# Performance work log

Hardware: AMD Instinct MI355X
Metric: run time of the kernel (lower is better)

Reference implementation:

```python
import jax, jax.numpy as jnp
import numpy as np

B, S, D, H, E, N = 4, 1024, 1024, 4096, 1024, 8


def setup_inputs() -> dict:
    key = jax.random.key(0)
    ks = jax.random.split(key, 5)
    x = jax.random.normal(ks[0], (B, S, D), jnp.float32)
    # Learned parameters (Linear weights stored as [in, out] for x @ W)
    Wg = jax.random.normal(ks[1], (D, N), jnp.float32) * 0.02
    bg = jnp.zeros((N,), jnp.float32)
    W1 = jax.random.normal(ks[2], (N, D, H), jnp.float32) * 0.02
    b1 = jnp.zeros((N, H), jnp.float32)
    W2 = jax.random.normal(ks[3], (N, H, E), jnp.float32) * 0.02
    b2 = jnp.zeros((N, E), jnp.float32)
    return {"x": x, "Wg": Wg, "bg": bg, "W1": W1, "b1": b1,
            "W2": W2, "b2": b2, "num_experts_per_tok": 2}


def reference(x, Wg, bg, W1, b1, W2, b2, num_experts_per_tok):
    # Gating: softmax over experts
    gate_probs = jax.nn.softmax(x @ Wg + bg, axis=-1)            # [B,S,N]
    n_exp = gate_probs.shape[-1]
    # Top-k routing mask (indices are distinct, so summed one-hots == scatter of 1.0)
    _, topk_idx = jax.lax.top_k(gate_probs, num_experts_per_tok)  # [B,S,k]
    mask = jax.nn.one_hot(topk_idx, n_exp, dtype=gate_probs.dtype).sum(axis=-2)  # [B,S,N]
    gated = gate_probs * mask
    # F.normalize(p=1): divide by max(L1-norm, eps)
    gated = gated / jnp.maximum(jnp.sum(jnp.abs(gated), axis=-1, keepdims=True), 1e-12)
    # Dense all-expert FFN (matches torch.stack over ModuleList)
    h = jax.nn.relu(jnp.einsum('bsd,ndh->bsnh', x, W1) + b1)      # [B,S,N,H]
    expert_out = jnp.einsum('bsnh,nhe->bsne', h, W2) + b2          # [B,S,N,E]
    out = jnp.einsum('bsn,bsne->bse', gated, expert_out)           # [B,S,E]
    # Auxiliary load-balancing stats
    tokens = float(x.shape[0] * x.shape[1])
    importance = gate_probs.sum(axis=(0, 1)) / tokens              # [N]
    load = mask.sum(axis=(0, 1)) / tokens                          # [N]
    lb_loss = (n_exp * (importance * load).sum()).astype(out.dtype)
    return out, lb_loss, importance, load
```

## Files before the change

### kernel.cpp

```cpp
#include <hip/hip_runtime.h>

#define TOKENS 4096
#define DDIM 1024
#define HDIM 4096
#define EDIM 1024
#define NEXP 8
#define SLOTS (TOKENS * 2)
#define OUT_MAIN ((size_t)TOKENS * EDIM)
#define NKC2 2
#define KCHUNK2 (HDIM / NKC2)

typedef __bf16 bf16_t;
typedef bf16_t bf16x8 __attribute__((ext_vector_type(8)));
typedef float f32x4 __attribute__((ext_vector_type(4)));

__device__ __forceinline__ unsigned short f32_to_bf16(float f) {
  union { float f; unsigned u; } v; v.f = f;
  unsigned r = v.u + 0x7FFFu + ((v.u >> 16) & 1u);
  return (unsigned short)(r >> 16);
}

__device__ __forceinline__ void gload_lds16(const void* g, void* l) {
  __builtin_amdgcn_global_load_lds(
      (__attribute__((address_space(1))) void*)(g),
      (__attribute__((address_space(3))) void*)(l), 16, 0, 0);
}

__global__ __launch_bounds__(256) void gate_kernel(
    const float* __restrict__ x, const float* __restrict__ Wg,
    const float* __restrict__ bg, unsigned short* __restrict__ xb,
    int2* __restrict__ tok_e, float2* __restrict__ tok_w,
    float* __restrict__ probs) {
  const int wave = threadIdx.x >> 6;
  const int lane = threadIdx.x & 63;
  const int t = blockIdx.x * 4 + wave;
  const float4* xr = reinterpret_cast<const float4*>(x + (size_t)t * DDIM);
  ushort4* xbr = reinterpret_cast<ushort4*>(xb + (size_t)t * DDIM);

  float acc[NEXP];
#pragma unroll
  for (int n = 0; n < NEXP; n++) acc[n] = 0.f;

#pragma unroll
  for (int i = 0; i < 4; i++) {
    int d4 = lane + 64 * i;
    float4 xv = xr[d4];
    ushort4 o;
    o.x = f32_to_bf16(xv.x); o.y = f32_to_bf16(xv.y);
    o.z = f32_to_bf16(xv.z); o.w = f32_to_bf16(xv.w);
    xbr[d4] = o;
    const float* wrow = Wg + (size_t)d4 * 4 * NEXP;
#pragma unroll
    for (int n = 0; n < NEXP; n++)
      acc[n] += xv.x * wrow[n] + xv.y * wrow[NEXP + n] +
                xv.z * wrow[2 * NEXP + n] + xv.w * wrow[3 * NEXP + n];
  }
#pragma unroll
  for (int n = 0; n < NEXP; n++)
#pragma unroll
    for (int m = 32; m > 0; m >>= 1) acc[n] += __shfl_xor(acc[n], m, 64);

  if (lane == 0) {
    float p[NEXP];
    float mx = -1e30f;
#pragma unroll
    for (int n = 0; n < NEXP; n++) { p[n] = acc[n] + bg[n]; mx = fmaxf(mx, p[n]); }
    float s = 0.f;
#pragma unroll
    for (int n = 0; n < NEXP; n++) { p[n] = expf(p[n] - mx); s += p[n]; }
    float inv = 1.f / s;
#pragma unroll
    for (int n = 0; n < NEXP; n++) { p[n] *= inv; probs[(size_t)t * NEXP + n] = p[n]; }
    int e1 = 0; float p1 = p[0];
#pragma unroll
    for (int n = 1; n < NEXP; n++) if (p[n] > p1) { p1 = p[n]; e1 = n; }
    int e2 = (e1 == 0) ? 1 : 0; float p2 = p[e2];
#pragma unroll
    for (int n = 0; n < NEXP; n++) if (n != e1 && p[n] > p2) { p2 = p[n]; e2 = n; }
    float denom = p1 + p2;
    tok_e[t] = make_int2(e1, e2);
    tok_w[t] = make_float2(p1 / denom, p2 / denom);
  }
}

__global__ __launch_bounds__(1024) void route_kernel(
    const int2* __restrict__ tok_e, const float2* __restrict__ tok_w,
    int* __restrict__ offs_g, int* __restrict__ counts_g,
    int* __restrict__ token_ids, float* __restrict__ slot_w) {
  __shared__ int cnt[NEXP];
  __shared__ int offs[NEXP + 1];
  __shared__ int cur[NEXP];
  const int tid = threadIdx.x;
  if (tid < NEXP) cnt[tid] = 0;
  __syncthreads();
  int2 e[4]; float2 w[4];
#pragma unroll
  for (int i = 0; i < 4; i++) {
    int t = tid + 1024 * i;
    e[i] = tok_e[t]; w[i] = tok_w[t];
    atomicAdd(&cnt[e[i].x], 1);
    atomicAdd(&cnt[e[i].y], 1);
  }
  __syncthreads();
  if (tid == 0) {
    int s = 0;
#pragma unroll
    for (int n = 0; n < NEXP; n++) { offs[n] = s; cur[n] = s; s += cnt[n]; }
    offs[NEXP] = s;
  }
  __syncthreads();
  if (tid < NEXP) { offs_g[tid] = offs[tid]; counts_g[tid] = cnt[tid]; }
  if (tid == 0) offs_g[NEXP] = offs[NEXP];
#pragma unroll
  for (int i = 0; i < 4; i++) {
    int t = tid + 1024 * i;
    int s0 = atomicAdd(&cur[e[i].x], 1);
    token_ids[s0] = t; slot_w[s0] = w[i].x;
    int s1 = atomicAdd(&cur[e[i].y], 1);
    token_ids[s1] = t; slot_w[s1] = w[i].y;
  }
}

__global__ __launch_bounds__(256) void transpose_convert_kernel(
    const float* __restrict__ src, unsigned short* __restrict__ dst, int R, int C) {
  __shared__ float tile[64][65];
  const size_t mat = (size_t)R * C;
  const float* s = src + (size_t)blockIdx.z * mat;
  unsigned short* d = dst + (size_t)blockIdx.z * mat;
  int c0 = blockIdx.x * 64, r0 = blockIdx.y * 64;
  int tx = threadIdx.x & 15, ty = threadIdx.x >> 4;
#pragma unroll
  for (int i = 0; i < 4; i++) {
    int row = ty + 16 * i;
    float4 v = *reinterpret_cast<const float4*>(&s[(size_t)(r0 + row) * C + c0 + tx * 4]);
    tile[row][tx * 4 + 0] = v.x;
    tile[row][tx * 4 + 1] = v.y;
    tile[row][tx * 4 + 2] = v.z;
    tile[row][tx * 4 + 3] = v.w;
  }
  __syncthreads();
#pragma unroll
  for (int i = 0; i < 4; i++) {
    int col = ty + 16 * i;
    ushort4 o;
    o.x = f32_to_bf16(tile[tx * 4 + 0][col]);
    o.y = f32_to_bf16(tile[tx * 4 + 1][col]);
    o.z = f32_to_bf16(tile[tx * 4 + 2][col]);
    o.w = f32_to_bf16(tile[tx * 4 + 3][col]);
    *reinterpret_cast<ushort4*>(&d[(size_t)(c0 + col) * R + r0 + tx * 4]) = o;
  }
}

__global__ __launch_bounds__(256) void gemm1_kernel(
    const unsigned short* __restrict__ xb, const unsigned short* __restrict__ w1t,
    const float* __restrict__ b1, const int* __restrict__ token_ids,
    const int* __restrict__ offs, unsigned short* __restrict__ h) {
  const int e = blockIdx.z;
  const int off0 = offs[e];
  const int ne = offs[e + 1] - off0;
  const int mt = blockIdx.y;
  if (mt * 128 >= ne) return;
  const int nt = blockIdx.x;

  __shared__ unsigned short As[2][128 * 64];
  __shared__ unsigned short Bs[2][128 * 64];

  const int tid = threadIdx.x;
  const int lane = tid & 63;
  const int wave = tid >> 6;
  const int wm = (wave >> 1) * 64;
  const int wn = (wave & 1) * 64;

  const int prow = tid >> 3;
  const int krow = (tid & 7) ^ (prow & 7);
  const unsigned short* gA[4];
  const unsigned short* gB[4];
  const unsigned short* wbase = w1t + (size_t)e * HDIM * DDIM;
#pragma unroll
  for (int j = 0; j < 4; j++) {
    int row = prow + j * 32;
    int slot = off0 + min(mt * 128 + row, ne - 1);
    gA[j] = xb + (size_t)token_ids[slot] * DDIM + krow * 8;
    gB[j] = wbase + (size_t)(nt * 128 + row) * DDIM + krow * 8;
  }

  f32x4 acc[4][4];
#pragma unroll
  for (int i = 0; i < 4; i++)
#pragma unroll
    for (int j = 0; j < 4; j++) acc[i][j] = (f32x4)(0.f);

  const int frow = lane & 15;
  const int q = lane >> 4;
  const int NK = DDIM / 64;

#pragma unroll
  for (int j = 0; j < 4; j++) {
    gload_lds16(gA[j], &As[0][j * 2048 + wave * 512]);
    gload_lds16(gB[j], &Bs[0][j * 2048 + wave * 512]);
  }
  __syncthreads();

  for (int t = 0; t < NK; t++) {
    const int cur = t & 1;
    if (t + 1 < NK) {
      const int k1 = (t + 1) * 64;
#pragma unroll
      for (int j = 0; j < 4; j++) {
        gload_lds16(gA[j] + k1, &As[cur ^ 1][j * 2048 + wave * 512]);
        gload_lds16(gB[j] + k1, &Bs[cur ^ 1][j * 2048 + wave * 512]);
      }
    }
#pragma unroll
    for (int kk = 0; kk < 2; kk++) {
      bf16x8 af[4], bfv[4];
#pragma unroll
      for (int mi = 0; mi < 4; mi++) {
        int row = wm + mi * 16 + frow;
        int k16 = (kk * 4 + q) ^ (row & 7);
        af[mi] = *reinterpret_cast<const bf16x8*>(&As[cur][row * 64 + k16 * 8]);
      }
#pragma unroll
      for (int ni = 0; ni < 4; ni++) {
        int row = wn + ni * 16 + frow;
        int k16 = (kk * 4 + q) ^ (row & 7);
        bfv[ni] = *reinterpret_cast<const bf16x8*>(&Bs[cur][row * 64 + k16 * 8]);
      }
#pragma unroll
      for (int mi = 0; mi < 4; mi++)
#pragma unroll
        for (int ni = 0; ni < 4; ni++)
          acc[mi][ni] = __builtin_amdgcn_mfma_f32_16x16x32_bf16(af[mi], bfv[ni], acc[mi][ni], 0, 0, 0);
    }
    __syncthreads();
  }

  const float* b1e = b1 + (size_t)e * HDIM + nt * 128;
  const int r4 = (lane >> 4) * 4;
  const int cb = lane & 15;
#pragma unroll
  for (int mi = 0; mi < 4; mi++) {
#pragma unroll
    for (int r = 0; r < 4; r++) {
      int grow = mt * 128 + wm + mi * 16 + r4 + r;
      if (grow < ne) {
        unsigned short* hr = h + (size_t)(off0 + grow) * HDIM + nt * 128;
#pragma unroll
        for (int ni = 0; ni < 4; ni++) {
          int col = wn + ni * 16 + cb;
          float v = acc[mi][ni][r] + b1e[col];
          hr[col] = f32_to_bf16(fmaxf(v, 0.f));
        }
      }
    }
  }
}

__global__ __launch_bounds__(256) void gemm2_kernel(
    const unsigned short* __restrict__ h, const unsigned short* __restrict__ w2t,
    const float* __restrict__ b2, const int* __restrict__ token_ids,
    const float* __restrict__ slot_w, const int* __restrict__ offs,
    float* __restrict__ out) {
  const int ez = blockIdx.z;
  const int e = ez >> 1;
  const int kc = ez & 1;
  const int off0 = offs[e];
  const int ne = offs[e + 1] - off0;
  const int mt = blockIdx.y;
  if (mt * 128 >= ne) return;
  const int nt = blockIdx.x;

  __shared__ unsigned short As[2][128 * 64];
  __shared__ unsigned short Bs[2][128 * 64];

  const int tid = threadIdx.x;
  const int lane = tid & 63;
  const int wave = tid >> 6;
  const int wm = (wave >> 1) * 64;
  const int wn = (wave & 1) * 64;

  const int prow = tid >> 3;
  const int krow = (tid & 7) ^ (prow & 7);
  const unsigned short* gA[4];
  const unsigned short* gB[4];
  const unsigned short* wbase = w2t + (size_t)e * EDIM * HDIM;
  const int kbase = kc * KCHUNK2;
#pragma unroll
  for (int j = 0; j < 4; j++) {
    int row = prow + j * 32;
    int slot = off0 + min(mt * 128 + row, ne - 1);
    gA[j] = h + (size_t)slot * HDIM + kbase + krow * 8;
    gB[j] = wbase + (size_t)(nt * 128 + row) * HDIM + kbase + krow * 8;
  }

  f32x4 acc[4][4];
#pragma unroll
  for (int i = 0; i < 4; i++)
#pragma unroll
    for (int j = 0; j < 4; j++) acc[i][j] = (f32x4)(0.f);

  const int frow = lane & 15;
  const int q = lane >> 4;
  const int NK = KCHUNK2 / 64;

#pragma unroll
  for (int j = 0; j < 4; j++) {
    gload_lds16(gA[j], &As[0][j * 2048 + wave * 512]);
    gload_lds16(gB[j], &Bs[0][j * 2048 + wave * 512]);
  }
  __syncthreads();

  for (int t = 0; t < NK; t++) {
    const int cur = t & 1;
    if (t + 1 < NK) {
      const int k1 = (t + 1) * 64;
#pragma unroll
      for (int j = 0; j < 4; j++) {
        gload_lds16(gA[j] + k1, &As[cur ^ 1][j * 2048 + wave * 512]);
        gload_lds16(gB[j] + k1, &Bs[cur ^ 1][j * 2048 + wave * 512]);
      }
    }
#pragma unroll
    for (int kk = 0; kk < 2; kk++) {
      bf16x8 af[4], bfv[4];
#pragma unroll
      for (int mi = 0; mi < 4; mi++) {
        int row = wm + mi * 16 + frow;
        int k16 = (kk * 4 + q) ^ (row & 7);
        af[mi] = *reinterpret_cast<const bf16x8*>(&As[cur][row * 64 + k16 * 8]);
      }
#pragma unroll
      for (int ni = 0; ni < 4; ni++) {
        int row = wn + ni * 16 + frow;
        int k16 = (kk * 4 + q) ^ (row & 7);
        bfv[ni] = *reinterpret_cast<const bf16x8*>(&Bs[cur][row * 64 + k16 * 8]);
      }
#pragma unroll
      for (int mi = 0; mi < 4; mi++)
#pragma unroll
        for (int ni = 0; ni < 4; ni++)
          acc[mi][ni] = __builtin_amdgcn_mfma_f32_16x16x32_bf16(af[mi], bfv[ni], acc[mi][ni], 0, 0, 0);
    }
    __syncthreads();
  }

  const float* b2e = b2 + (size_t)e * EDIM + nt * 128;
  const int r4 = (lane >> 4) * 4;
  const int cb = lane & 15;
#pragma unroll
  for (int mi = 0; mi < 4; mi++) {
#pragma unroll
    for (int r = 0; r < 4; r++) {
      int grow = mt * 128 + wm + mi * 16 + r4 + r;
      if (grow < ne) {
        int slot = off0 + grow;
        int tokid = token_ids[slot];
        float wgt = slot_w[slot];
        float* orow = out + (size_t)tokid * EDIM + nt * 128;
#pragma unroll
        for (int ni = 0; ni < 4; ni++) {
          int col = wn + ni * 16 + cb;
          float bias = (kc == 0) ? b2e[col] : 0.f;
          atomicAdd(&orow[col], (acc[mi][ni][r] + bias) * wgt);
        }
      }
    }
  }
}

__global__ __launch_bounds__(512) void stats_kernel(
    const float* __restrict__ probs, const int* __restrict__ counts,
    float* __restrict__ tail) {
  const int wave = threadIdx.x >> 6;
  const int lane = threadIdx.x & 63;
  float s = 0.f;
  for (int t = lane; t < TOKENS; t += 64) s += probs[(size_t)t * NEXP + wave];
#pragma unroll
  for (int m = 32; m > 0; m >>= 1) s += __shfl_xor(s, m, 64);
  __shared__ float imp_s[NEXP];
  if (lane == 0) imp_s[wave] = s / (float)TOKENS;
  __syncthreads();
  if (threadIdx.x == 0) {
    float lb = 0.f;
#pragma unroll
    for (int n = 0; n < NEXP; n++) {
      float imp = imp_s[n];
      float ld = (float)counts[n] / (float)TOKENS;
      tail[1 + n] = imp;
      tail[1 + NEXP + n] = ld;
      lb += imp * ld;
    }
    tail[0] = (float)NEXP * lb;
  }
}

extern "C" void kernel_launch(void* const* d_in, const int* in_sizes, int n_in,
                              void* d_out, int out_size, void* d_ws, size_t ws_size,
                              hipStream_t stream) {
  const float* x  = (const float*)d_in[0];
  const float* Wg = (const float*)d_in[1];
  const float* bg = (const float*)d_in[2];
  const float* W1 = (const float*)d_in[3];
  const float* b1 = (const float*)d_in[4];
  const float* W2 = (const float*)d_in[5];
  const float* b2 = (const float*)d_in[6];
  float* out = (float*)d_out;
  char* ws = (char*)d_ws;

  const size_t XB_OFF   = 0;
  const size_t W1T_OFF  = XB_OFF + (size_t)TOKENS * DDIM * 2;
  const size_t W2T_OFF  = W1T_OFF + (size_t)NEXP * DDIM * HDIM * 2;
  const size_t H_OFF    = W2T_OFF + (size_t)NEXP * HDIM * EDIM * 2;
  const size_t TOKE_OFF = H_OFF + (size_t)SLOTS * HDIM * 2;
  const size_t TOKW_OFF = TOKE_OFF + (size_t)TOKENS * sizeof(int2);
  const size_t TID_OFF  = TOKW_OFF + (size_t)TOKENS * sizeof(float2);
  const size_t SLW_OFF  = TID_OFF + (size_t)SLOTS * 4;
  const size_t PROB_OFF = SLW_OFF + (size_t)SLOTS * 4;
  const size_t META_OFF = PROB_OFF + (size_t)TOKENS * NEXP * 4;
  const size_t WS_NEED  = META_OFF + 64 * 4;
  if (ws_size < WS_NEED) return;

  unsigned short* xb   = (unsigned short*)(ws + XB_OFF);
  unsigned short* w1t  = (unsigned short*)(ws + W1T_OFF);
  unsigned short* w2t  = (unsigned short*)(ws + W2T_OFF);
  unsigned short* hbuf = (unsigned short*)(ws + H_OFF);
  int2*   tok_e = (int2*)(ws + TOKE_OFF);
  float2* tok_w = (float2*)(ws + TOKW_OFF);
  int*    tids  = (int*)(ws + TID_OFF);
  float*  slw   = (float*)(ws + SLW_OFF);
  float*  probs = (float*)(ws + PROB_OFF);
  int*    counts = (int*)(ws + META_OFF);
  int*    offs   = counts + 8;

  hipMemsetAsync(out, 0, (size_t)out_size * sizeof(float), stream);

  gate_kernel<<<TOKENS / 4, 256, 0, stream>>>(x, Wg, bg, xb, tok_e, tok_w, probs);
  route_kernel<<<1, 1024, 0, stream>>>(tok_e, tok_w, offs, counts, tids, slw);
  transpose_convert_kernel<<<dim3(HDIM / 64, DDIM / 64, NEXP), 256, 0, stream>>>(W1, w1t, DDIM, HDIM);
  transpose_convert_kernel<<<dim3(EDIM / 64, HDIM / 64, NEXP), 256, 0, stream>>>(W2, w2t, HDIM, EDIM);
  gemm1_kernel<<<dim3(HDIM / 128, SLOTS / 128, NEXP), 256, 0, stream>>>(xb, w1t, b1, tids, offs, hbuf);
  gemm2_kernel<<<dim3(EDIM / 128, SLOTS / 128, NEXP * NKC2), 256, 0, stream>>>(hbuf, w2t, b2, tids, slw, offs, out);
  stats_kernel<<<1, 512, 0, stream>>>(probs, counts, out + OUT_MAIN);
}
```

Baseline: 495.0 us.

## Deepen GEMM prefetch pipeline with register-staged LDS reads and vmcnt waits

Both expert GEMM kernels now prefetch two K-tiles ahead. Each iteration loads the whole current LDS tile into registers, releases the buffer with a barrier, then issues the global-to-LDS load for tile t+2 into that buffer before running the MFMAs. Explicit vmcnt waits replace the full __syncthreads, so global loads can overlap more compute. The MFMA block is also raised in priority with s_setprio. The cost is more registers for the fragments and an extra barrier per iteration, and the hand-written vmcnt counts must match the number of loads in flight.

```diff
diff --git a/kernel.cpp b/kernel.cpp
--- a/kernel.cpp
+++ b/kernel.cpp
@@ -194,45 +194,52 @@
   const int q = lane >> 4;
   const int NK = DDIM / 64;
 
-#pragma unroll
-  for (int j = 0; j < 4; j++) {
-    gload_lds16(gA[j], &As[0][j * 2048 + wave * 512]);
-    gload_lds16(gB[j], &Bs[0][j * 2048 + wave * 512]);
-  }
-  __syncthreads();
+  auto stage = [&](int tt, int buf) {
+#pragma unroll
+    for (int j = 0; j < 4; j++) {
+      gload_lds16(gA[j] + tt * 64, &As[buf][j * 2048 + wave * 512]);
+      gload_lds16(gB[j] + tt * 64, &Bs[buf][j * 2048 + wave * 512]);
+    }
+  };
+
+  stage(0, 0);
+  stage(1, 1);
 
   for (int t = 0; t < NK; t++) {
     const int cur = t & 1;
-    if (t + 1 < NK) {
-      const int k1 = (t + 1) * 64;
-#pragma unroll
-      for (int j = 0; j < 4; j++) {
-        gload_lds16(gA[j] + k1, &As[cur ^ 1][j * 2048 + wave * 512]);
-        gload_lds16(gB[j] + k1, &Bs[cur ^ 1][j * 2048 + wave * 512]);
-      }
-    }
+    if (t == NK - 1) asm volatile("s_waitcnt vmcnt(0)" ::: "memory");
+    else             asm volatile("s_waitcnt vmcnt(8)" ::: "memory");
+    __builtin_amdgcn_s_barrier();
+
+    bf16x8 af[2][4], bfv[2][4];
 #pragma unroll
     for (int kk = 0; kk < 2; kk++) {
-      bf16x8 af[4], bfv[4];
 #pragma unroll
       for (int mi = 0; mi < 4; mi++) {
         int row = wm + mi * 16 + frow;
         int k16 = (kk * 4 + q) ^ (row & 7);
-        af[mi] = *reinterpret_cast<const bf16x8*>(&As[cur][row * 64 + k16 * 8]);
+        af[kk][mi] = *reinterpret_cast<const bf16x8*>(&As[cur][row * 64 + k16 * 8]);
       }
 #pragma unroll
       for (int ni = 0; ni < 4; ni++) {
         int row = wn + ni * 16 + frow;
         int k16 = (kk * 4 + q) ^ (row & 7);
-        bfv[ni] = *reinterpret_cast<const bf16x8*>(&Bs[cur][row * 64 + k16 * 8]);
-      }
+        bfv[kk][ni] = *reinterpret_cast<const bf16x8*>(&Bs[cur][row * 64 + k16 * 8]);
+      }
+    }
+    asm volatile("s_waitcnt lgkmcnt(0)" ::: "memory");
+    __builtin_amdgcn_s_barrier();
+    if (t + 2 < NK) stage(t + 2, cur);
+
+    __builtin_amdgcn_s_setprio(1);
+#pragma unroll
+    for (int kk = 0; kk < 2; kk++)
 #pragma unroll
       for (int mi = 0; mi < 4; mi++)
 #pragma unroll
         for (int ni = 0; ni < 4; ni++)
-          acc[mi][ni] = __builtin_amdgcn_mfma_f32_16x16x32_bf16(af[mi], bfv[ni], acc[mi][ni], 0, 0, 0);
-    }
-    __syncthreads();
+          acc[mi][ni] = __builtin_amdgcn_mfma_f32_16x16x32_bf16(af[kk][mi], bfv[kk][ni], acc[mi][ni], 0, 0, 0);
+    __builtin_amdgcn_s_setprio(0);
   }
 
   const float* b1e = b1 + (size_t)e * HDIM + nt * 128;
@@ -303,45 +310,52 @@
   const int q = lane >> 4;
   const int NK = KCHUNK2 / 64;
 
-#pragma unroll
-  for (int j = 0; j < 4; j++) {
-    gload_lds16(gA[j], &As[0][j * 2048 + wave * 512]);
-    gload_lds16(gB[j], &Bs[0][j * 2048 + wave * 512]);
-  }
-  __syncthreads();
+  auto stage = [&](int tt, int buf) {
+#pragma unroll
+    for (int j = 0; j < 4; j++) {
+      gload_lds16(gA[j] + tt * 64, &As[buf][j * 2048 + wave * 512]);
+      gload_lds16(gB[j] + tt * 64, &Bs[buf][j * 2048 + wave * 512]);
+    }
+  };
+
+  stage(0, 0);
+  stage(1, 1);
 
   for (int t = 0; t < NK; t++) {
     const int cur = t & 1;
-    if (t + 1 < NK) {
-      const int k1 = (t + 1) * 64;
-#pragma unroll
-      for (int j = 0; j < 4; j++) {
-        gload_lds16(gA[j] + k1, &As[cur ^ 1][j * 2048 + wave * 512]);
-        gload_lds16(gB[j] + k1, &Bs[cur ^ 1][j * 2048 + wave * 512]);
-      }
-    }
+    if (t == NK - 1) asm volatile("s_waitcnt vmcnt(0)" ::: "memory");
+    else             asm volatile("s_waitcnt vmcnt(8)" ::: "memory");
+    __builtin_amdgcn_s_barrier();
+
+    bf16x8 af[2][4], bfv[2][4];
 #pragma unroll
     for (int kk = 0; kk < 2; kk++) {
-      bf16x8 af[4], bfv[4];
 #pragma unroll
       for (int mi = 0; mi < 4; mi++) {
         int row = wm + mi * 16 + frow;
         int k16 = (kk * 4 + q) ^ (row & 7);
-        af[mi] = *reinterpret_cast<const bf16x8*>(&As[cur][row * 64 + k16 * 8]);
+        af[kk][mi] = *reinterpret_cast<const bf16x8*>(&As[cur][row * 64 + k16 * 8]);
       }
 #pragma unroll
       for (int ni = 0; ni < 4; ni++) {
         int row = wn + ni * 16 + frow;
         int k16 = (kk * 4 + q) ^ (row & 7);
-        bfv[ni] = *reinterpret_cast<const bf16x8*>(&Bs[cur][row * 64 + k16 * 8]);
-      }
+        bfv[kk][ni] = *reinterpret_cast<const bf16x8*>(&Bs[cur][row * 64 + k16 * 8]);
+      }
+    }
+    asm volatile("s_waitcnt lgkmcnt(0)" ::: "memory");
+    __builtin_amdgcn_s_barrier();
+    if (t + 2 < NK) stage(t + 2, cur);
+
+    __builtin_amdgcn_s_setprio(1);
+#pragma unroll
+    for (int kk = 0; kk < 2; kk++)
 #pragma unroll
       for (int mi = 0; mi < 4; mi++)
 #pragma unroll
         for (int ni = 0; ni < 4; ni++)
-          acc[mi][ni] = __builtin_amdgcn_mfma_f32_16x16x32_bf16(af[mi], bfv[ni], acc[mi][ni], 0, 0, 0);
-    }
-    __syncthreads();
+          acc[mi][ni] = __builtin_amdgcn_mfma_f32_16x16x32_bf16(af[kk][mi], bfv[kk][ni], acc[mi][ni], 0, 0, 0);
+    __builtin_amdgcn_s_setprio(0);
   }
 
   const float* b2e = b2 + (size_t)e * EDIM + nt * 128;
```

New measurement: 436.4 us. -11.8%, faster.
